# Kernel tuning notes

Measured on AMD Instinct MI355X. Metric: run time of the kernel, lower is better.

The kernel has to match this reference:

```python
import jax, jax.numpy as jnp
import numpy as np

B, I, HID, H, KS = 64, 1024, 2048, 8, 4
D = HID // H  # head_size = 256; also BlockDiagonal block size = (2*I)//H = 256
EPS = 1e-5


def setup_inputs() -> dict:
    key = jax.random.key(0)
    ks = jax.random.split(key, 16)
    r = lambda i, shape, s=0.02: jax.random.normal(ks[i], shape, dtype=jnp.float32) * s
    z = lambda shape: jnp.zeros(shape, jnp.float32)
    return {
        "x": jax.random.normal(ks[0], (B, I), dtype=jnp.float32),
        "h_prev": z((B, H, D)),
        "c_prev": z((B, H, D, D)),
        "n_prev": z((B, H, D)),
        "m_prev": z((B, H)),
        "ln_w": jnp.ones((I,), jnp.float32), "ln_b": z((I,)),
        "W_ul": r(1, (I, HID)), "b_ul": z((HID,)),
        "W_ur": r(2, (I, HID)), "b_ur": z((HID,)),
        "W_conv": r(3, (HID, HID, KS)), "b_conv": z((HID,)),
        "W_skip": r(4, (HID, HID)), "b_skip": z((HID,)),
        "W_q": r(5, (H, D, D)), "b_q": z((HID,)),
        "W_k": r(6, (H, D, D)), "b_k": z((HID,)),
        "W_v": r(7, (H, D, D)), "b_v": z((HID,)),
        "W_i": r(8, (HID, H)), "b_i": z((H,)),
        "W_f": r(9, (HID, H)), "b_f": z((H,)),
        "W_o": r(10, (HID, HID)), "b_o": z((HID,)),
        "W_down": r(11, (HID, I)), "b_down": z((I,)),
        "gn_w": jnp.ones((HID,), jnp.float32), "gn_b": z((HID,)),
    }


def _block_diag(zf, W, b):
    # BlockDiagonal: chunk last dim into H blocks, per-block Linear, concat -> [B,H,D]
    zh = zf.reshape(zf.shape[0], H, -1)
    return jnp.einsum('bhi,hio->bho', zh, W) + b.reshape(H, -1)


def reference(x, h_prev, c_prev, n_prev, m_prev, ln_w, ln_b, W_ul, b_ul, W_ur, b_ur,
              W_conv, b_conv, W_skip, b_skip, W_q, b_q, W_k, b_k, W_v, b_v,
              W_i, b_i, W_f, b_f, W_o, b_o, W_down, b_down, gn_w, gn_b):
    # LayerNorm
    mu = x.mean(-1, keepdims=True)
    var = jnp.mean((x - mu) ** 2, -1, keepdims=True)
    xn = (x - mu) * jax.lax.rsqrt(var + EPS) * ln_w + ln_b
    # Up projections
    xl = xn @ W_ul + b_ul            # [B, 2I] == [B, HID]
    xr = xn @ W_ur + b_ur
    # Causal conv over a length-1 sequence: after left padding + slicing, only the
    # last kernel tap (index KS-1) touches real data -> linear map with W_conv[:,:,KS-1]
    xc = jax.nn.silu(xl @ W_conv[:, :, KS - 1].T + b_conv)
    x_skip = xc @ W_skip + b_skip    # [B, HID]
    q = _block_diag(xc, W_q, b_q)                       # [B,H,D]
    k = _block_diag(xc, W_k, b_k) / jnp.sqrt(jnp.float32(D))
    v = _block_diag(xl, W_v, b_v)
    i_t = xc @ W_i + b_i             # [B,H]
    f_t = xc @ W_f + b_f
    o = jax.nn.sigmoid(xl @ W_o + b_o).reshape(-1, H, D)
    # Stabilized exponential gating
    m_t = jnp.maximum(f_t + m_prev, i_t)
    i_g = jnp.exp(i_t - m_t)
    f_g = jnp.exp(f_t + m_prev - m_t)
    # Outer-product state update + bilinear readout
    c_t = f_g[..., None, None] * c_prev + i_g[..., None, None] * jnp.einsum('bhd,bhk->bhdk', v, k)
    n_t = f_g[..., None] * n_prev + i_g[..., None] * k
    num = jnp.einsum('bhdk,bhk->bhd', c_t, q)
    den = jnp.clip(jnp.einsum('bhd,bhd->bh', n_t, q), 1.0, None)[..., None]
    h_t = o * num / den              # [B,H,D]
    # GroupNorm with num_groups == num_heads: normalize per head
    g_mu = h_t.mean(-1, keepdims=True)
    g_var = jnp.mean((h_t - g_mu) ** 2, -1, keepdims=True)
    gn = ((h_t - g_mu) * jax.lax.rsqrt(g_var + EPS)).reshape(-1, HID) * gn_w + gn_b
    out = (gn + x_skip) * jax.nn.silu(xr)
    out = out @ W_down + b_down
    final = out + x
    return (final, h_t, c_t, n_t, m_t)
```

## Files before the change

### kernel.cpp

```cpp
#include <hip/hip_runtime.h>
#include <cstddef>

typedef __bf16 bf16;
typedef __bf16 bf16x8 __attribute__((ext_vector_type(8)));
typedef short  s16x8  __attribute__((ext_vector_type(8)));
typedef float  f32x4  __attribute__((ext_vector_type(4)));

template <class T> T&& declv() noexcept;
template <class, class = void> struct takes_bf16vec { static constexpr bool value = false; };
template <class V> struct takes_bf16vec<V, decltype((void)__builtin_amdgcn_mfma_f32_16x16x32_bf16(
    declv<V>(), declv<V>(), declv<f32x4>(), 0, 0, 0))> { static constexpr bool value = true; };

template <class V>
__device__ __forceinline__ f32x4 mfma_bf16_16x16x32(V a, V b, f32x4 c) {
  if constexpr (takes_bf16vec<V>::value) {
    return __builtin_amdgcn_mfma_f32_16x16x32_bf16(a, b, c, 0, 0, 0);
  } else {
    return __builtin_amdgcn_mfma_f32_16x16x32_bf16(
        __builtin_bit_cast(s16x8, a), __builtin_bit_cast(s16x8, b), c, 0, 0, 0);
  }
}

constexpr int M_NONE = 0, M_SILU = 1, M_SIG = 2;

__global__ __launch_bounds__(256) void ln_kernel(const float* __restrict__ x,
                                                 const float* __restrict__ w,
                                                 const float* __restrict__ bs,
                                                 const float* __restrict__ bdown,
                                                 bf16* __restrict__ xn,
                                                 float* __restrict__ outf) {
  const int b = blockIdx.x, tid = threadIdx.x;
  __shared__ float red[256];
  float vals[4];
  float s = 0.f;
#pragma unroll
  for (int i = 0; i < 4; ++i) { vals[i] = x[b * 1024 + i * 256 + tid]; s += vals[i]; }
  red[tid] = s; __syncthreads();
  for (int off = 128; off; off >>= 1) { if (tid < off) red[tid] += red[tid + off]; __syncthreads(); }
  const float mu = red[0] * (1.f / 1024.f);
  __syncthreads();
  float s2 = 0.f;
#pragma unroll
  for (int i = 0; i < 4; ++i) { const float d = vals[i] - mu; s2 += d * d; }
  red[tid] = s2; __syncthreads();
  for (int off = 128; off; off >>= 1) { if (tid < off) red[tid] += red[tid + off]; __syncthreads(); }
  const float rs = rsqrtf(red[0] * (1.f / 1024.f) + 1e-5f);
#pragma unroll
  for (int i = 0; i < 4; ++i) {
    const int j = i * 256 + tid;
    xn[b * 1024 + j] = (bf16)((vals[i] - mu) * rs * w[j] + bs[j]);
    outf[b * 1024 + j] = vals[i] + bdown[j];
  }
}

template <int K, int NW>
__device__ __forceinline__ void gemm_tile(
    const bf16* __restrict__ A, int ldA, int aOff,
    const float* __restrict__ W, int ldB, int wcol,
    const float* __restrict__ bias, int bOff, float scale, int mode,
    float* __restrict__ outF, bf16* __restrict__ outB, int outLd, int oOff,
    float lds[NW][64][20]) {
  const int tid = threadIdx.x;
  const int lane = tid & 63, wave = tid >> 6;
  const int l15 = lane & 15, quad = lane >> 4;
  constexpr int chunk = K / NW;
  const int kbeg = wave * chunk;
  f32x4 acc0{}, acc1{}, acc2{}, acc3{};
#pragma unroll 4
  for (int k = 0; k < chunk; k += 32) {
    const int kk = kbeg + k + quad * 8;
    bf16x8 bfrag;
    const float* wp = W + (size_t)kk * ldB + wcol + l15;
#pragma unroll
    for (int j = 0; j < 8; ++j) bfrag[j] = (bf16)wp[(size_t)j * ldB];
    const bf16* ap = A + (size_t)l15 * ldA + aOff + kk;
    const size_t st = (size_t)16 * ldA;
    bf16x8 a0 = *(const bf16x8*)(ap);
    bf16x8 a1 = *(const bf16x8*)(ap + st);
    bf16x8 a2 = *(const bf16x8*)(ap + 2 * st);
    bf16x8 a3 = *(const bf16x8*)(ap + 3 * st);
    acc0 = mfma_bf16_16x16x32(a0, bfrag, acc0);
    acc1 = mfma_bf16_16x16x32(a1, bfrag, acc1);
    acc2 = mfma_bf16_16x16x32(a2, bfrag, acc2);
    acc3 = mfma_bf16_16x16x32(a3, bfrag, acc3);
  }
#pragma unroll
  for (int r = 0; r < 4; ++r) {
    const int rr = quad * 4 + r;
    lds[wave][rr][l15]      = acc0[r];
    lds[wave][16 + rr][l15] = acc1[r];
    lds[wave][32 + rr][l15] = acc2[r];
    lds[wave][48 + rr][l15] = acc3[r];
  }
  __syncthreads();
  if (tid < 256) {
    const int col = tid & 15, rb = (tid >> 4) << 2;
    const float bvv = bias[bOff + col];
#pragma unroll
    for (int r2 = 0; r2 < 4; ++r2) {
      const int row = rb + r2;
      float v = bvv;
#pragma unroll
      for (int w = 0; w < NW; ++w) v += lds[w][row][col];
      v *= scale;
      if (mode == M_SILU)      v = v / (1.f + expf(-v));
      else if (mode == M_SIG)  v = 1.f / (1.f + expf(-v));
      const size_t oi = (size_t)row * outLd + oOff + col;
      if (outF) outF[oi] = v;
      if (outB) outB[oi] = (bf16)v;
    }
  }
}

__global__ __launch_bounds__(512) void gemm_ulur(
    const bf16* __restrict__ xn,
    const float* __restrict__ W_ul, const float* __restrict__ W_ur,
    const float* __restrict__ b_ul, const float* __restrict__ b_ur,
    bf16* __restrict__ xl_bf, float* __restrict__ xr_f) {
  __shared__ float lds[8][64][20];
  const int l = (blockIdx.x & 7) * 32 + (blockIdx.x >> 3);
  const int ncol = (l & 127) * 16;
  if (l >> 7) {
    gemm_tile<1024, 8>(xn, 1024, 0, W_ur, 2048, ncol, b_ur, ncol, 1.f, M_NONE,
                       xr_f, nullptr, 2048, ncol, lds);
  } else {
    gemm_tile<1024, 8>(xn, 1024, 0, W_ul, 2048, ncol, b_ul, ncol, 1.f, M_NONE,
                       nullptr, xl_bf, 2048, ncol, lds);
  }
}

__global__ __launch_bounds__(512) void gemm_conv(
    const bf16* __restrict__ xl, const float* __restrict__ Wc,
    const float* __restrict__ bc, bf16* __restrict__ xc) {
  __shared__ float lds[8][64][20];
  const int tid = threadIdx.x;
  const int lane = tid & 63, wave = tid >> 6;
  const int l15 = lane & 15, quad = lane >> 4;
  const int n0 = blockIdx.x * 8;
  const int kbeg = wave * 256;
  f32x4 acc0{}, acc1{}, acc2{}, acc3{};
#pragma unroll 4
  for (int k = 0; k < 256; k += 32) {
    const int kk = kbeg + k + quad * 8;
    bf16x8 bfrag;
    const float* wp = Wc + ((size_t)(n0 + (l15 & 7)) * 2048 + kk) * 4 + 3;
#pragma unroll
    for (int j = 0; j < 8; ++j) bfrag[j] = (bf16)wp[j * 4];
    const bf16* ap = xl + (size_t)l15 * 2048 + kk;
    const size_t st = (size_t)16 * 2048;
    bf16x8 a0 = *(const bf16x8*)(ap);
    bf16x8 a1 = *(const bf16x8*)(ap + st);
    bf16x8 a2 = *(const bf16x8*)(ap + 2 * st);
    bf16x8 a3 = *(const bf16x8*)(ap + 3 * st);
    acc0 = mfma_bf16_16x16x32(a0, bfrag, acc0);
    acc1 = mfma_bf16_16x16x32(a1, bfrag, acc1);
    acc2 = mfma_bf16_16x16x32(a2, bfrag, acc2);
    acc3 = mfma_bf16_16x16x32(a3, bfrag, acc3);
  }
#pragma unroll
  for (int r = 0; r < 4; ++r) {
    const int rr = quad * 4 + r;
    lds[wave][rr][l15]      = acc0[r];
    lds[wave][16 + rr][l15] = acc1[r];
    lds[wave][32 + rr][l15] = acc2[r];
    lds[wave][48 + rr][l15] = acc3[r];
  }
  __syncthreads();
  if (tid < 128) {
    const int col = tid & 7, rb = (tid >> 3) << 2;
    const float bvv = bc[n0 + col];
#pragma unroll
    for (int r2 = 0; r2 < 4; ++r2) {
      const int row = rb + r2;
      float v = bvv;
#pragma unroll
      for (int w = 0; w < 8; ++w) v += lds[w][row][col];
      v = v / (1.f + expf(-v));
      xc[(size_t)row * 2048 + n0 + col] = (bf16)v;
    }
  }
}

__global__ __launch_bounds__(256) void mega_c(
    const bf16* __restrict__ xc, const bf16* __restrict__ xl,
    const float* __restrict__ W_skip, const float* __restrict__ b_skip,
    const float* __restrict__ W_o, const float* __restrict__ b_o,
    const float* __restrict__ Wq, const float* __restrict__ bq,
    const float* __restrict__ Wk, const float* __restrict__ bk,
    const float* __restrict__ Wv, const float* __restrict__ bv,
    const float* __restrict__ Wi, const float* __restrict__ bi,
    const float* __restrict__ Wf, const float* __restrict__ bfv,
    const float* __restrict__ m_prev,
    float* __restrict__ xskip_f, float* __restrict__ o_f,
    float* __restrict__ qf, float* __restrict__ kf, float* __restrict__ vf,
    float* __restrict__ ig, float* __restrict__ fgo, float* __restrict__ mt_out) {
  __shared__ float lds[4][64][20];
  const int bid = (blockIdx.x & 7) * 88 + (blockIdx.x >> 3);
  if (bid < 256) {
    const int seg = bid >> 7, ncol = (bid & 127) * 16;
    if (seg) {
      gemm_tile<2048, 4>(xl, 2048, 0, W_o, 2048, ncol, b_o, ncol, 1.f, M_SIG,
                         o_f, nullptr, 2048, ncol, lds);
    } else {
      gemm_tile<2048, 4>(xc, 2048, 0, W_skip, 2048, ncol, b_skip, ncol, 1.f, M_NONE,
                         xskip_f, nullptr, 2048, ncol, lds);
    }
  } else if (bid < 640) {
    const int t6 = bid - 256;
    const int seg = t6 >> 7, t = t6 & 127;
    const int n0 = t * 16, h = t >> 4;
    const bf16* A = (seg == 2) ? xl : xc;
    const float* W = (seg == 0) ? Wq : (seg == 1) ? Wk : Wv;
    const float* bias = (seg == 0) ? bq : (seg == 1) ? bk : bv;
    float* out = (seg == 0) ? qf : (seg == 1) ? kf : vf;
    gemm_tile<256, 4>(A, 2048, h << 8, W + (size_t)h * 65536, 256, n0 & 255,
                      bias, n0, (seg == 1) ? 0.0625f : 1.f, M_NONE,
                      out, nullptr, 2048, n0, lds);
  } else {
    const int b = bid - 640, tid = threadIdx.x;
    float* shf = &lds[0][0][0];
    float (*ri)[8] = reinterpret_cast<float(*)[8]>(shf);
    float (*rf)[8] = reinterpret_cast<float(*)[8]>(shf + 2048);
    float ai[8] = {}, af[8] = {};
    for (int k = tid; k < 2048; k += 256) {
      const float xv = (float)xc[b * 2048 + k];
      const float4 wi0 = *(const float4*)(Wi + (size_t)k * 8);
      const float4 wi1 = *(const float4*)(Wi + (size_t)k * 8 + 4);
      const float4 wf0 = *(const float4*)(Wf + (size_t)k * 8);
      const float4 wf1 = *(const float4*)(Wf + (size_t)k * 8 + 4);
      ai[0] += xv * wi0.x; ai[1] += xv * wi0.y; ai[2] += xv * wi0.z; ai[3] += xv * wi0.w;
      ai[4] += xv * wi1.x; ai[5] += xv * wi1.y; ai[6] += xv * wi1.z; ai[7] += xv * wi1.w;
      af[0] += xv * wf0.x; af[1] += xv * wf0.y; af[2] += xv * wf0.z; af[3] += xv * wf0.w;
      af[4] += xv * wf1.x; af[5] += xv * wf1.y; af[6] += xv * wf1.z; af[7] += xv * wf1.w;
    }
#pragma unroll
    for (int h = 0; h < 8; ++h) { ri[tid][h] = ai[h]; rf[tid][h] = af[h]; }
    __syncthreads();
    for (int off = 128; off; off >>= 1) {
      if (tid < off) {
#pragma unroll
        for (int h = 0; h < 8; ++h) { ri[tid][h] += ri[tid + off][h]; rf[tid][h] += rf[tid + off][h]; }
      }
      __syncthreads();
    }
    if (tid < 8) {
      const float it = ri[0][tid] + bi[tid];
      const float ft = rf[0][tid] + bfv[tid];
      const float mp = m_prev[b * 8 + tid];
      const float mt = fmaxf(ft + mp, it);
      mt_out[b * 8 + tid] = mt;
      ig[b * 8 + tid] = expf(it - mt);
      fgo[b * 8 + tid] = expf(ft + mp - mt);
    }
  }
}

__global__ __launch_bounds__(256) void state_fused(
    const float* __restrict__ c_prev, const float* __restrict__ n_prev,
    const float* __restrict__ qf, const float* __restrict__ kf,
    const float* __restrict__ vf, const float* __restrict__ of,
    const float* __restrict__ ig, const float* __restrict__ fg,
    const float* __restrict__ xskip, const float* __restrict__ xrf,
    const float* __restrict__ gnw, const float* __restrict__ gnb,
    float* __restrict__ ct_out, float* __restrict__ nt_out,
    float* __restrict__ ht_out, bf16* __restrict__ pre_bf) {
  const int bh = blockIdx.x, b = bh >> 3, h = bh & 7;
  const int tid = threadIdx.x;
  const int vb = b * 2048 + h * 256;
  __shared__ float q_s[256], k_s[256], num_s[256], red[256];
  q_s[tid] = qf[vb + tid];
  k_s[tid] = kf[vb + tid];
  const float i_g = ig[bh], f_g = fg[bh];
  __syncthreads();
  const int lane8 = tid & 7, rowbase = tid >> 3;
#pragma unroll
  for (int rg = 0; rg < 8; ++rg) {
    const int row = rg * 32 + rowbase;
    const float iv = i_g * vf[vb + row];
    const size_t base = ((size_t)bh << 16) + ((size_t)row << 8) + lane8 * 4;
    float p = 0.f;
#pragma unroll
    for (int i = 0; i < 8; ++i) {
      const int c = lane8 * 4 + i * 32;
      const float4 cp = *(const float4*)(c_prev + base + i * 32);
      float4 cn;
      cn.x = f_g * cp.x + iv * k_s[c];
      cn.y = f_g * cp.y + iv * k_s[c + 1];
      cn.z = f_g * cp.z + iv * k_s[c + 2];
      cn.w = f_g * cp.w + iv * k_s[c + 3];
      *(float4*)(ct_out + base + i * 32) = cn;
      p += cn.x * q_s[c] + cn.y * q_s[c + 1] + cn.z * q_s[c + 2] + cn.w * q_s[c + 3];
    }
    p += __shfl_xor(p, 1, 64);
    p += __shfl_xor(p, 2, 64);
    p += __shfl_xor(p, 4, 64);
    if (lane8 == 0) num_s[row] = p;
  }
  __syncthreads();
  const float qv = q_s[tid], kv = k_s[tid];
  const float nv = f_g * n_prev[bh * 256 + tid] + i_g * kv;
  nt_out[bh * 256 + tid] = nv;
  red[tid] = nv * qv;
  __syncthreads();
  for (int off = 128; off; off >>= 1) { if (tid < off) red[tid] += red[tid + off]; __syncthreads(); }
  const float den = fmaxf(red[0], 1.0f);
  const float hv = of[vb + tid] * num_s[tid] / den;
  ht_out[bh * 256 + tid] = hv;
  __syncthreads();
  red[tid] = hv; __syncthreads();
  for (int off = 128; off; off >>= 1) { if (tid < off) red[tid] += red[tid + off]; __syncthreads(); }
  const float mu = red[0] * (1.f / 256.f);
  __syncthreads();
  const float dv = hv - mu;
  red[tid] = dv * dv; __syncthreads();
  for (int off = 128; off; off >>= 1) { if (tid < off) red[tid] += red[tid + off]; __syncthreads(); }
  const float gn = (hv - mu) * rsqrtf(red[0] * (1.f / 256.f) + 1e-5f);
  const int j = h * 256 + tid;
  const float xr = xrf[b * 2048 + j];
  const float pre = (gn * gnw[j] + gnb[j] + xskip[b * 2048 + j]) * (xr / (1.f + expf(-xr)));
  pre_bf[b * 2048 + j] = (bf16)pre;
}

template <int K, int KS, int NTILES>
__global__ __launch_bounds__(256) void gemm_atomic(
    const bf16* __restrict__ A, const float* __restrict__ W,
    int ldA, int ldB, float* __restrict__ dst, int outN) {
  constexpr int Kslice = K / KS;
  constexpr int chunk = Kslice / 4;
  const int tid = threadIdx.x;
  const int lane = tid & 63, wave = tid >> 6;
  const int l15 = lane & 15, quad = lane >> 4;
  const int l = (blockIdx.x & 7) * ((NTILES * KS) / 8) + (blockIdx.x >> 3);
  const int tile = l % NTILES, ks = l / NTILES;
  const int ncol = tile * 16;
  const int kbeg = ks * Kslice + wave * chunk;

  f32x4 acc0{}, acc1{}, acc2{}, acc3{};
#pragma unroll
  for (int k = 0; k < chunk; k += 32) {
    const int kk = kbeg + k + quad * 8;
    bf16x8 bfrag;
    const float* wp = W + (size_t)kk * ldB + ncol + l15;
#pragma unroll
    for (int j = 0; j < 8; ++j) bfrag[j] = (bf16)wp[(size_t)j * ldB];
    const bf16* ap = A + (size_t)l15 * ldA + kk;
    const size_t st = (size_t)16 * ldA;
    bf16x8 a0 = *(const bf16x8*)(ap);
    bf16x8 a1 = *(const bf16x8*)(ap + st);
    bf16x8 a2 = *(const bf16x8*)(ap + 2 * st);
    bf16x8 a3 = *(const bf16x8*)(ap + 3 * st);
    acc0 = mfma_bf16_16x16x32(a0, bfrag, acc0);
    acc1 = mfma_bf16_16x16x32(a1, bfrag, acc1);
    acc2 = mfma_bf16_16x16x32(a2, bfrag, acc2);
    acc3 = mfma_bf16_16x16x32(a3, bfrag, acc3);
  }
  __shared__ float lds[4][64][20];
#pragma unroll
  for (int r = 0; r < 4; ++r) {
    const int rr = quad * 4 + r;
    lds[wave][rr][l15]      = acc0[r];
    lds[wave][16 + rr][l15] = acc1[r];
    lds[wave][32 + rr][l15] = acc2[r];
    lds[wave][48 + rr][l15] = acc3[r];
  }
  __syncthreads();
  const int col = tid & 15, rb = (tid >> 4) << 2;
#pragma unroll
  for (int r2 = 0; r2 < 4; ++r2) {
    const int row = rb + r2;
    const float v = lds[0][row][col] + lds[1][row][col] + lds[2][row][col] + lds[3][row][col];
    atomicAdd(dst + (size_t)row * outN + ncol + col, v);
  }
}

extern "C" void kernel_launch(void* const* d_in, const int* in_sizes, int n_in,
                              void* d_out, int out_size, void* d_ws, size_t ws_size,
                              hipStream_t stream) {
  (void)in_sizes; (void)n_in; (void)out_size; (void)ws_size;
  const float* x      = (const float*)d_in[0];
  const float* c_prev = (const float*)d_in[2];
  const float* n_prev = (const float*)d_in[3];
  const float* m_prev = (const float*)d_in[4];
  const float* ln_w = (const float*)d_in[5];
  const float* ln_b = (const float*)d_in[6];
  const float* W_ul = (const float*)d_in[7];
  const float* b_ul = (const float*)d_in[8];
  const float* W_ur = (const float*)d_in[9];
  const float* b_ur = (const float*)d_in[10];
  const float* W_conv = (const float*)d_in[11];
  const float* b_conv = (const float*)d_in[12];
  const float* W_skip = (const float*)d_in[13];
  const float* b_skip = (const float*)d_in[14];
  const float* W_q = (const float*)d_in[15];
  const float* b_q = (const float*)d_in[16];
  const float* W_k = (const float*)d_in[17];
  const float* b_k = (const float*)d_in[18];
  const float* W_v = (const float*)d_in[19];
  const float* b_v = (const float*)d_in[20];
  const float* W_i = (const float*)d_in[21];
  const float* b_i = (const float*)d_in[22];
  const float* W_f = (const float*)d_in[23];
  const float* b_f = (const float*)d_in[24];
  const float* W_o = (const float*)d_in[25];
  const float* b_o = (const float*)d_in[26];
  const float* W_down = (const float*)d_in[27];
  const float* b_down = (const float*)d_in[28];
  const float* gn_w = (const float*)d_in[29];
  const float* gn_b = (const float*)d_in[30];

  float* out_final = (float*)d_out;
  float* out_ht = out_final + 65536;
  float* out_ct = out_final + 196608;
  float* out_nt = out_final + 33751040;
  float* out_mt = out_final + 33882112;

  char* ws = (char*)d_ws;
  bf16*  xn_bf   = (bf16*)(ws + 0);
  bf16*  xl_bf   = (bf16*)(ws + 131072);
  bf16*  xc_bf   = (bf16*)(ws + 393216);
  bf16*  pre_bf  = (bf16*)(ws + 655360);
  float* xr_f    = (float*)(ws + 917504);
  float* xskip_f = (float*)(ws + 1441792);
  float* q_f     = (float*)(ws + 1966080);
  float* k_f     = (float*)(ws + 2490368);
  float* v_f     = (float*)(ws + 3014656);
  float* o_f     = (float*)(ws + 3538944);
  float* ig_f    = (float*)(ws + 4063232);
  float* fg_f    = (float*)(ws + 4065280);

  ln_kernel<<<64, 256, 0, stream>>>(x, ln_w, ln_b, b_down, xn_bf, out_final);
  gemm_ulur<<<256, 512, 0, stream>>>(xn_bf, W_ul, W_ur, b_ul, b_ur, xl_bf, xr_f);
  gemm_conv<<<256, 512, 0, stream>>>(xl_bf, W_conv, b_conv, xc_bf);
  mega_c<<<704, 256, 0, stream>>>(
      xc_bf, xl_bf, W_skip, b_skip, W_o, b_o, W_q, b_q, W_k, b_k, W_v, b_v,
      W_i, b_i, W_f, b_f, m_prev, xskip_f, o_f, q_f, k_f, v_f, ig_f, fg_f, out_mt);
  state_fused<<<512, 256, 0, stream>>>(
      c_prev, n_prev, q_f, k_f, v_f, o_f, ig_f, fg_f,
      xskip_f, xr_f, gn_w, gn_b, out_ct, out_nt, out_ht, pre_bf);
  gemm_atomic<2048, 8, 64><<<512, 256, 0, stream>>>(
      pre_bf, W_down, 2048, 1024, out_final, 1024);
}
```

Before: 442.2 us.

## Move W_o GEMM into conv kernel, shrink GEMM blocks, use nontemporal state access

Moves the sigmoid W_o projection out of mega_c into a new conv_o kernel so it runs alongside the conv GEMM and rebalances work across launches. The up-projection and conv GEMMs drop from 8 to 4 waves per block, each wave covering a longer K chunk. The large c_prev/c_t streams in state_fused switch to nontemporal loads and stores to avoid polluting caches. The XCD-aware block index swizzles are removed, which may change L2 locality of weight reads.

```diff
diff --git a/kernel.cpp b/kernel.cpp
--- a/kernel.cpp
+++ b/kernel.cpp
@@ -22,6 +22,14 @@
 }
 
 constexpr int M_NONE = 0, M_SILU = 1, M_SIG = 2;
+
+__device__ __forceinline__ float4 nt_load4(const float* p) {
+  f32x4 v = __builtin_nontemporal_load((const f32x4*)p);
+  return *(float4*)&v;
+}
+__device__ __forceinline__ void nt_store4(float* p, float4 v) {
+  __builtin_nontemporal_store(*(f32x4*)&v, (f32x4*)p);
+}
 
 __global__ __launch_bounds__(256) void ln_kernel(const float* __restrict__ x,
                                                  const float* __restrict__ w,
@@ -53,17 +61,17 @@
   }
 }
 
-template <int K, int NW>
+template <int K>
 __device__ __forceinline__ void gemm_tile(
     const bf16* __restrict__ A, int ldA, int aOff,
     const float* __restrict__ W, int ldB, int wcol,
     const float* __restrict__ bias, int bOff, float scale, int mode,
     float* __restrict__ outF, bf16* __restrict__ outB, int outLd, int oOff,
-    float lds[NW][64][20]) {
+    float lds[4][64][20]) {
   const int tid = threadIdx.x;
   const int lane = tid & 63, wave = tid >> 6;
   const int l15 = lane & 15, quad = lane >> 4;
-  constexpr int chunk = K / NW;
+  constexpr int chunk = K / 4;
   const int kbeg = wave * chunk;
   f32x4 acc0{}, acc1{}, acc2{}, acc3{};
 #pragma unroll 4
@@ -93,54 +101,58 @@
     lds[wave][48 + rr][l15] = acc3[r];
   }
   __syncthreads();
-  if (tid < 256) {
-    const int col = tid & 15, rb = (tid >> 4) << 2;
-    const float bvv = bias[bOff + col];
-#pragma unroll
-    for (int r2 = 0; r2 < 4; ++r2) {
-      const int row = rb + r2;
-      float v = bvv;
-#pragma unroll
-      for (int w = 0; w < NW; ++w) v += lds[w][row][col];
-      v *= scale;
-      if (mode == M_SILU)      v = v / (1.f + expf(-v));
-      else if (mode == M_SIG)  v = 1.f / (1.f + expf(-v));
-      const size_t oi = (size_t)row * outLd + oOff + col;
-      if (outF) outF[oi] = v;
-      if (outB) outB[oi] = (bf16)v;
-    }
-  }
-}
-
-__global__ __launch_bounds__(512) void gemm_ulur(
+  const int col = tid & 15, rb = (tid >> 4) << 2;
+  const float bvv = bias[bOff + col];
+#pragma unroll
+  for (int r2 = 0; r2 < 4; ++r2) {
+    const int row = rb + r2;
+    float v = (lds[0][row][col] + lds[1][row][col] + lds[2][row][col] + lds[3][row][col] + bvv) * scale;
+    if (mode == M_SILU)      v = v / (1.f + expf(-v));
+    else if (mode == M_SIG)  v = 1.f / (1.f + expf(-v));
+    const size_t oi = (size_t)row * outLd + oOff + col;
+    if (outF) outF[oi] = v;
+    if (outB) outB[oi] = (bf16)v;
+  }
+}
+
+__global__ __launch_bounds__(256) void gemm_ulur(
     const bf16* __restrict__ xn,
     const float* __restrict__ W_ul, const float* __restrict__ W_ur,
     const float* __restrict__ b_ul, const float* __restrict__ b_ur,
     bf16* __restrict__ xl_bf, float* __restrict__ xr_f) {
-  __shared__ float lds[8][64][20];
-  const int l = (blockIdx.x & 7) * 32 + (blockIdx.x >> 3);
-  const int ncol = (l & 127) * 16;
-  if (l >> 7) {
-    gemm_tile<1024, 8>(xn, 1024, 0, W_ur, 2048, ncol, b_ur, ncol, 1.f, M_NONE,
-                       xr_f, nullptr, 2048, ncol, lds);
+  __shared__ float lds[4][64][20];
+  const int tile = blockIdx.x;
+  const int ncol = (tile & 127) * 16;
+  if (tile >> 7) {
+    gemm_tile<1024>(xn, 1024, 0, W_ur, 2048, ncol, b_ur, ncol, 1.f, M_NONE,
+                    xr_f, nullptr, 2048, ncol, lds);
   } else {
-    gemm_tile<1024, 8>(xn, 1024, 0, W_ul, 2048, ncol, b_ul, ncol, 1.f, M_NONE,
-                       nullptr, xl_bf, 2048, ncol, lds);
-  }
-}
-
-__global__ __launch_bounds__(512) void gemm_conv(
+    gemm_tile<1024>(xn, 1024, 0, W_ul, 2048, ncol, b_ul, ncol, 1.f, M_NONE,
+                    nullptr, xl_bf, 2048, ncol, lds);
+  }
+}
+
+__global__ __launch_bounds__(256) void conv_o(
     const bf16* __restrict__ xl, const float* __restrict__ Wc,
-    const float* __restrict__ bc, bf16* __restrict__ xc) {
-  __shared__ float lds[8][64][20];
+    const float* __restrict__ bc,
+    const float* __restrict__ W_o, const float* __restrict__ b_o,
+    bf16* __restrict__ xc, float* __restrict__ o_f) {
+  __shared__ float lds[4][64][20];
+  const int bid = blockIdx.x;
+  if (bid >= 256) {
+    const int ncol = (bid - 256) * 16;
+    gemm_tile<2048>(xl, 2048, 0, W_o, 2048, ncol, b_o, ncol, 1.f, M_SIG,
+                    o_f, nullptr, 2048, ncol, lds);
+    return;
+  }
   const int tid = threadIdx.x;
   const int lane = tid & 63, wave = tid >> 6;
   const int l15 = lane & 15, quad = lane >> 4;
-  const int n0 = blockIdx.x * 8;
-  const int kbeg = wave * 256;
+  const int n0 = bid * 8;
+  const int kbeg = wave * 512;
   f32x4 acc0{}, acc1{}, acc2{}, acc3{};
 #pragma unroll 4
-  for (int k = 0; k < 256; k += 32) {
+  for (int k = 0; k < 512; k += 32) {
     const int kk = kbeg + k + quad * 8;
     bf16x8 bfrag;
     const float* wp = Wc + ((size_t)(n0 + (l15 & 7)) * 2048 + kk) * 4 + 3;
@@ -172,9 +184,7 @@
 #pragma unroll
     for (int r2 = 0; r2 < 4; ++r2) {
       const int row = rb + r2;
-      float v = bvv;
-#pragma unroll
-      for (int w = 0; w < 8; ++w) v += lds[w][row][col];
+      float v = lds[0][row][col] + lds[1][row][col] + lds[2][row][col] + lds[3][row][col] + bvv;
       v = v / (1.f + expf(-v));
       xc[(size_t)row * 2048 + n0 + col] = (bf16)v;
     }
@@ -184,40 +194,34 @@
 __global__ __launch_bounds__(256) void mega_c(
     const bf16* __restrict__ xc, const bf16* __restrict__ xl,
     const float* __restrict__ W_skip, const float* __restrict__ b_skip,
-    const float* __restrict__ W_o, const float* __restrict__ b_o,
     const float* __restrict__ Wq, const float* __restrict__ bq,
     const float* __restrict__ Wk, const float* __restrict__ bk,
     const float* __restrict__ Wv, const float* __restrict__ bv,
     const float* __restrict__ Wi, const float* __restrict__ bi,
     const float* __restrict__ Wf, const float* __restrict__ bfv,
     const float* __restrict__ m_prev,
-    float* __restrict__ xskip_f, float* __restrict__ o_f,
+    float* __restrict__ xskip_f,
     float* __restrict__ qf, float* __restrict__ kf, float* __restrict__ vf,
     float* __restrict__ ig, float* __restrict__ fgo, float* __restrict__ mt_out) {
   __shared__ float lds[4][64][20];
-  const int bid = (blockIdx.x & 7) * 88 + (blockIdx.x >> 3);
-  if (bid < 256) {
-    const int seg = bid >> 7, ncol = (bid & 127) * 16;
-    if (seg) {
-      gemm_tile<2048, 4>(xl, 2048, 0, W_o, 2048, ncol, b_o, ncol, 1.f, M_SIG,
-                         o_f, nullptr, 2048, ncol, lds);
-    } else {
-      gemm_tile<2048, 4>(xc, 2048, 0, W_skip, 2048, ncol, b_skip, ncol, 1.f, M_NONE,
-                         xskip_f, nullptr, 2048, ncol, lds);
-    }
-  } else if (bid < 640) {
-    const int t6 = bid - 256;
+  const int bid = blockIdx.x;
+  if (bid < 128) {
+    const int ncol = bid * 16;
+    gemm_tile<2048>(xc, 2048, 0, W_skip, 2048, ncol, b_skip, ncol, 1.f, M_NONE,
+                    xskip_f, nullptr, 2048, ncol, lds);
+  } else if (bid < 512) {
+    const int t6 = bid - 128;
     const int seg = t6 >> 7, t = t6 & 127;
     const int n0 = t * 16, h = t >> 4;
     const bf16* A = (seg == 2) ? xl : xc;
     const float* W = (seg == 0) ? Wq : (seg == 1) ? Wk : Wv;
     const float* bias = (seg == 0) ? bq : (seg == 1) ? bk : bv;
     float* out = (seg == 0) ? qf : (seg == 1) ? kf : vf;
-    gemm_tile<256, 4>(A, 2048, h << 8, W + (size_t)h * 65536, 256, n0 & 255,
-                      bias, n0, (seg == 1) ? 0.0625f : 1.f, M_NONE,
-                      out, nullptr, 2048, n0, lds);
+    gemm_tile<256>(A, 2048, h << 8, W + (size_t)h * 65536, 256, n0 & 255,
+                   bias, n0, (seg == 1) ? 0.0625f : 1.f, M_NONE,
+                   out, nullptr, 2048, n0, lds);
   } else {
-    const int b = bid - 640, tid = threadIdx.x;
+    const int b = bid - 512, tid = threadIdx.x;
     float* shf = &lds[0][0][0];
     float (*ri)[8] = reinterpret_cast<float(*)[8]>(shf);
     float (*rf)[8] = reinterpret_cast<float(*)[8]>(shf + 2048);
@@ -282,13 +286,13 @@
 #pragma unroll
     for (int i = 0; i < 8; ++i) {
       const int c = lane8 * 4 + i * 32;
-      const float4 cp = *(const float4*)(c_prev + base + i * 32);
+      const float4 cp = nt_load4(c_prev + base + i * 32);
       float4 cn;
       cn.x = f_g * cp.x + iv * k_s[c];
       cn.y = f_g * cp.y + iv * k_s[c + 1];
       cn.z = f_g * cp.z + iv * k_s[c + 2];
       cn.w = f_g * cp.w + iv * k_s[c + 3];
-      *(float4*)(ct_out + base + i * 32) = cn;
+      nt_store4(ct_out + base + i * 32, cn);
       p += cn.x * q_s[c] + cn.y * q_s[c + 1] + cn.z * q_s[c + 2] + cn.w * q_s[c + 3];
     }
     p += __shfl_xor(p, 1, 64);
@@ -330,8 +334,7 @@
   const int tid = threadIdx.x;
   const int lane = tid & 63, wave = tid >> 6;
   const int l15 = lane & 15, quad = lane >> 4;
-  const int l = (blockIdx.x & 7) * ((NTILES * KS) / 8) + (blockIdx.x >> 3);
-  const int tile = l % NTILES, ks = l / NTILES;
+  const int tile = blockIdx.x % NTILES, ks = blockIdx.x / NTILES;
   const int ncol = tile * 16;
   const int kbeg = ks * Kslice + wave * chunk;
 
@@ -429,11 +432,11 @@
   float* fg_f    = (float*)(ws + 4065280);
 
   ln_kernel<<<64, 256, 0, stream>>>(x, ln_w, ln_b, b_down, xn_bf, out_final);
-  gemm_ulur<<<256, 512, 0, stream>>>(xn_bf, W_ul, W_ur, b_ul, b_ur, xl_bf, xr_f);
-  gemm_conv<<<256, 512, 0, stream>>>(xl_bf, W_conv, b_conv, xc_bf);
-  mega_c<<<704, 256, 0, stream>>>(
-      xc_bf, xl_bf, W_skip, b_skip, W_o, b_o, W_q, b_q, W_k, b_k, W_v, b_v,
-      W_i, b_i, W_f, b_f, m_prev, xskip_f, o_f, q_f, k_f, v_f, ig_f, fg_f, out_mt);
+  gemm_ulur<<<256, 256, 0, stream>>>(xn_bf, W_ul, W_ur, b_ul, b_ur, xl_bf, xr_f);
+  conv_o<<<384, 256, 0, stream>>>(xl_bf, W_conv, b_conv, W_o, b_o, xc_bf, o_f);
+  mega_c<<<576, 256, 0, stream>>>(
+      xc_bf, xl_bf, W_skip, b_skip, W_q, b_q, W_k, b_k, W_v, b_v,
+      W_i, b_i, W_f, b_f, m_prev, xskip_f, q_f, k_f, v_f, ig_f, fg_f, out_mt);
   state_fused<<<512, 256, 0, stream>>>(
       c_prev, n_prev, q_f, k_f, v_f, o_f, ig_f, fg_f,
       xskip_f, xr_f, gn_w, gn_b, out_ct, out_nt, out_ht, pre_bf);
```

Result: faster. 423.1 us (-4.3%).
